# Kernel tuning notes

Measured on AMD Instinct MI355X. Metric: run time of the kernel, lower is better.

## Reference

```python
import jax, jax.numpy as jnp
import numpy as np

B, T, F, U = 256, 2048, 64, 10  # batch, timesteps, features, lstm units


def setup_inputs() -> dict:
    key = jax.random.key(0)
    k1, k2, k3, k4 = jax.random.split(key, 4)
    return {
        "x": jax.random.normal(k1, (B, T, F), dtype=jnp.float32),
        "kernel": jax.random.normal(k2, (F, 4 * U), dtype=jnp.float32) * 0.1,
        "recurrent_kernel": jax.random.normal(k3, (U, 4 * U), dtype=jnp.float32) * 0.1,
        "bias": jnp.zeros((4 * U,), dtype=jnp.float32),
        "dense_w": jax.random.normal(k4, (U, 1), dtype=jnp.float32) * 0.1,
        "dense_b": jnp.zeros((1,), dtype=jnp.float32),
    }


def reference(x, kernel, recurrent_kernel, bias, dense_w, dense_b):
    units = recurrent_kernel.shape[0]
    batch = x.shape[0]
    # Precompute input contribution for all timesteps: [B, T, 4U]
    xz = jnp.einsum('btf,fg->btg', x, kernel) + bias

    def step(carry, z_t):
        h, c = carry
        z = z_t + h @ recurrent_kernel  # [B, 4U]
        i, f, g, o = jnp.split(z, 4, axis=-1)  # Keras gate order: i, f, c, o
        i = jax.nn.sigmoid(i)
        f = jax.nn.sigmoid(f)
        g = jax.nn.soft_sign(g)       # activation='softsign'
        o = jax.nn.sigmoid(o)
        c = f * c + i * g
        h = o * jax.nn.soft_sign(c)
        return (h, c), None

    h0 = jnp.zeros((batch, units), dtype=x.dtype)
    (h, _), _ = jax.lax.scan(step, (h0, h0), jnp.swapaxes(xz, 0, 1))
    logit = h @ dense_w + dense_b  # [B, 1]
    return jax.nn.sigmoid(logit)
```

## Files before the change

### kernel.cpp

```cpp
#include <hip/hip_runtime.h>

#define B_ 256
#define T_ 2048
#define F_ 64
#define U_ 10
#define G_ 40
#define CH 64
#define NCH (T_ / CH)
#define NLOG2E (-1.44269504088896340736f)

__device__ __forceinline__ float rcp_f(float x) { return __builtin_amdgcn_rcpf(x); }
__device__ __forceinline__ float exp2_f(float x) { return __builtin_amdgcn_exp2f(x); }
__device__ __forceinline__ float rdlane_f(float v, int l) {
  return __int_as_float(__builtin_amdgcn_readlane(__float_as_int(v), l));
}
template <int CTRL>
__device__ __forceinline__ float qbcast(float v) {
  return __int_as_float(
      __builtin_amdgcn_update_dpp(0, __float_as_int(v), CTRL, 0xF, 0xF, true));
}
__device__ __forceinline__ void gload_lds16(const float* g, float* l) {
  __builtin_amdgcn_global_load_lds(
      (const __attribute__((address_space(1))) void*)g,
      (__attribute__((address_space(3))) void*)l, 16, 0, 0);
}

__global__ __launch_bounds__(256, 1) void lstm_fused(
    const float* __restrict__ x, const float* __restrict__ W,
    const float* __restrict__ R, const float* __restrict__ bias,
    const float* __restrict__ dw, const float* __restrict__ db,
    float* __restrict__ out) {
  __shared__ float xb[2][CH * F_];
  __shared__ float zb[2][CH * G_];
  const int b = blockIdx.x;
  const int tid = threadIdx.x;
  const int wave = tid >> 6;
  const int lane = tid & 63;
  const float* xbase = x + (size_t)b * T_ * F_;

  if (wave == 0) {
    __builtin_amdgcn_s_setprio(3);
    const int L = (lane < G_) ? lane : (G_ - 1);
    const int u = L >> 2, gate = L & 3;
    const int col = gate * U_ + u;
    const float sc = (gate == 2) ? 1.f : NLOG2E;
    float Rc[U_];
    #pragma unroll
    for (int j = 0; j < U_; ++j) Rc[j] = R[j * G_ + col] * sc;
    const float dwu = dw[u];
    const float db0 = db[0];
    float h = 0.f, c = 0.f;

    auto step = [&](float zseed) {
      float h0 = rdlane_f(h, 0),  h1 = rdlane_f(h, 4),  h2 = rdlane_f(h, 8);
      float h3 = rdlane_f(h, 12), h4 = rdlane_f(h, 16), h5 = rdlane_f(h, 20);
      float h6 = rdlane_f(h, 24), h7 = rdlane_f(h, 28);
      float h8 = rdlane_f(h, 32), h9 = rdlane_f(h, 36);
      float q0 = fmaf(h0, Rc[0], zseed);
      q0 = fmaf(h1, Rc[1], q0);
      q0 = fmaf(h2, Rc[2], q0);
      float q1 = h3 * Rc[3];
      q1 = fmaf(h4, Rc[4], q1);
      q1 = fmaf(h5, Rc[5], q1);
      float q2 = h6 * Rc[6];
      q2 = fmaf(h7, Rc[7], q2);
      float q3 = h8 * Rc[8];
      q3 = fmaf(h9, Rc[9], q3);
      float zz = (q0 + q2) + (q1 + q3);
      float sg = rcp_f(1.f + exp2_f(zz));
      float ss = zz * rcp_f(1.f + __builtin_fabsf(zz));
      float a = (gate == 2) ? ss : sg;
      float ai = qbcast<0x00>(a);
      float af = qbcast<0x55>(a);
      float ag = qbcast<0xAA>(a);
      float ao = qbcast<0xFF>(a);
      c = fmaf(af, c, ai * ag);
      float oc = ao * c;
      float den = 1.f + __builtin_fabsf(c);
      h = oc * rcp_f(den);
    };

    __syncthreads();
    __syncthreads();
    for (int cc = 0; cc < NCH; ++cc) {
      const float* zp = zb[cc & 1] + L;
      float zA0 = zp[0 * G_], zA1 = zp[1 * G_], zA2 = zp[2 * G_], zA3 = zp[3 * G_];
      float zB0 = zp[4 * G_], zB1 = zp[5 * G_], zB2 = zp[6 * G_], zB3 = zp[7 * G_];
      #pragma unroll 1
      for (int pr = 0; pr < 8; ++pr) {
        const float* zn = zp + 8 * G_;
        const float* zs = (pr < 7) ? zn : zp;
        float c0 = zA0, c1 = zA1, c2 = zA2, c3 = zA3;
        zA0 = zs[0 * G_]; zA1 = zs[1 * G_];
        zA2 = zs[2 * G_]; zA3 = zs[3 * G_];
        step(c0); step(c1); step(c2); step(c3);
        float d0 = zB0, d1 = zB1, d2 = zB2, d3 = zB3;
        zB0 = zs[4 * G_]; zB1 = zs[5 * G_];
        zB2 = zs[6 * G_]; zB3 = zs[7 * G_];
        step(d0); step(d1); step(d2); step(d3);
        zp = zn;
      }
      __syncthreads();
    }
    float p = h * dwu;
    float logit = db0;
    #pragma unroll
    for (int j = 0; j < U_; ++j) logit += rdlane_f(p, 4 * j);
    if (lane == 0) out[b] = rcp_f(1.f + __expf(-logit));
  } else {
    const int p0 = tid - 64;
    const int p = (p0 < 160) ? p0 : 159;
    const bool act = (p0 < 160);
    const int s = p % G_;
    const int tsl = p / G_;
    const int u = s >> 2, gate = s & 3;
    const int col = gate * U_ + u;
    const int pw = wave - 1;
    const float scp = (gate == 2) ? 1.f : NLOG2E;
    float wc[F_];
    #pragma unroll
    for (int k = 0; k < F_; ++k) wc[k] = W[k * G_ + col];
    const float bcol = bias[col];

    auto load_x = [&](int cx) {
      const float* g = xbase + (size_t)cx * CH * F_;
      float* l = xb[cx & 1];
      for (int i = pw; i < 16; i += 3)
        gload_lds16(g + i * 256 + lane * 4, l + i * 256);
    };
    auto produce = [&](int tc) {
      const float* xr = xb[tc & 1];
      float* zrow = zb[tc & 1];
      for (int tt = tsl; tt < CH; tt += 4) {
        const float4* row4 = (const float4*)(xr + tt * F_);
        float z0 = bcol, z1 = 0.f, z2 = 0.f, z3 = 0.f;
        #pragma unroll
        for (int j = 0; j < 16; j += 4) {
          float4 a0 = row4[j], a1 = row4[j + 1], a2 = row4[j + 2], a3 = row4[j + 3];
          z0 = fmaf(a0.x, wc[4*j+0], z0);  z0 = fmaf(a0.y, wc[4*j+1], z0);
          z0 = fmaf(a0.z, wc[4*j+2], z0);  z0 = fmaf(a0.w, wc[4*j+3], z0);
          z1 = fmaf(a1.x, wc[4*j+4], z1);  z1 = fmaf(a1.y, wc[4*j+5], z1);
          z1 = fmaf(a1.z, wc[4*j+6], z1);  z1 = fmaf(a1.w, wc[4*j+7], z1);
          z2 = fmaf(a2.x, wc[4*j+8], z2);  z2 = fmaf(a2.y, wc[4*j+9], z2);
          z2 = fmaf(a2.z, wc[4*j+10], z2); z2 = fmaf(a2.w, wc[4*j+11], z2);
          z3 = fmaf(a3.x, wc[4*j+12], z3); z3 = fmaf(a3.y, wc[4*j+13], z3);
          z3 = fmaf(a3.z, wc[4*j+14], z3); z3 = fmaf(a3.w, wc[4*j+15], z3);
        }
        if (act) zrow[tt * G_ + s] = ((z0 + z1) + (z2 + z3)) * scp;
      }
    };

    load_x(0);
    load_x(1);
    __syncthreads();
    produce(0);
    __syncthreads();
    for (int cc = 0; cc < NCH; ++cc) {
      if (cc + 2 < NCH) load_x(cc + 2);
      if (cc + 1 < NCH) produce(cc + 1);
      __syncthreads();
    }
  }
}

extern "C" void kernel_launch(void* const* d_in, const int* in_sizes, int n_in,
                              void* d_out, int out_size, void* d_ws, size_t ws_size,
                              hipStream_t stream) {
  const float* x    = (const float*)d_in[0];
  const float* W    = (const float*)d_in[1];
  const float* R    = (const float*)d_in[2];
  const float* bias = (const float*)d_in[3];
  const float* dw   = (const float*)d_in[4];
  const float* db   = (const float*)d_in[5];
  float* out = (float*)d_out;
  (void)d_ws; (void)ws_size; (void)in_sizes; (void)n_in; (void)out_size;
  lstm_fused<<<B_, 256, 0, stream>>>(x, W, R, bias, dw, db, out);
}
```

Measured before the change: 358.6 us.

## Process two batch sequences per block to interleave independent recurrences

```diff
diff --git a/kernel.cpp b/kernel.cpp
--- a/kernel.cpp
+++ b/kernel.cpp
@@ -5,7 +5,7 @@
 #define F_ 64
 #define U_ 10
 #define G_ 40
-#define CH 64
+#define CH 32
 #define NCH (T_ / CH)
 #define NLOG2E (-1.44269504088896340736f)
 
@@ -30,13 +30,14 @@
     const float* __restrict__ R, const float* __restrict__ bias,
     const float* __restrict__ dw, const float* __restrict__ db,
     float* __restrict__ out) {
-  __shared__ float xb[2][CH * F_];
-  __shared__ float zb[2][CH * G_];
-  const int b = blockIdx.x;
+  __shared__ float xb[2][2][CH * F_];
+  __shared__ float2 zbuf[2][CH * G_];
+  const int blk = blockIdx.x;
   const int tid = threadIdx.x;
   const int wave = tid >> 6;
   const int lane = tid & 63;
-  const float* xbase = x + (size_t)b * T_ * F_;
+  const float* xA = x + (size_t)(2 * blk) * T_ * F_;
+  const float* xBp = x + (size_t)(2 * blk + 1) * T_ * F_;
 
   if (wave == 0) {
     __builtin_amdgcn_s_setprio(3);
@@ -49,64 +50,81 @@
     for (int j = 0; j < U_; ++j) Rc[j] = R[j * G_ + col] * sc;
     const float dwu = dw[u];
     const float db0 = db[0];
-    float h = 0.f, c = 0.f;
-
-    auto step = [&](float zseed) {
-      float h0 = rdlane_f(h, 0),  h1 = rdlane_f(h, 4),  h2 = rdlane_f(h, 8);
-      float h3 = rdlane_f(h, 12), h4 = rdlane_f(h, 16), h5 = rdlane_f(h, 20);
-      float h6 = rdlane_f(h, 24), h7 = rdlane_f(h, 28);
-      float h8 = rdlane_f(h, 32), h9 = rdlane_f(h, 36);
-      float q0 = fmaf(h0, Rc[0], zseed);
-      q0 = fmaf(h1, Rc[1], q0);
-      q0 = fmaf(h2, Rc[2], q0);
-      float q1 = h3 * Rc[3];
-      q1 = fmaf(h4, Rc[4], q1);
-      q1 = fmaf(h5, Rc[5], q1);
-      float q2 = h6 * Rc[6];
-      q2 = fmaf(h7, Rc[7], q2);
-      float q3 = h8 * Rc[8];
-      q3 = fmaf(h9, Rc[9], q3);
-      float zz = (q0 + q2) + (q1 + q3);
-      float sg = rcp_f(1.f + exp2_f(zz));
-      float ss = zz * rcp_f(1.f + __builtin_fabsf(zz));
-      float a = (gate == 2) ? ss : sg;
-      float ai = qbcast<0x00>(a);
-      float af = qbcast<0x55>(a);
-      float ag = qbcast<0xAA>(a);
-      float ao = qbcast<0xFF>(a);
-      c = fmaf(af, c, ai * ag);
-      float oc = ao * c;
-      float den = 1.f + __builtin_fabsf(c);
-      h = oc * rcp_f(den);
+    float hA = 0.f, cA = 0.f, hB = 0.f, cB = 0.f;
+
+    auto step2 = [&](float2 z2) {
+      float a0 = rdlane_f(hA, 0),  b0 = rdlane_f(hB, 0);
+      float a1 = rdlane_f(hA, 4),  b1 = rdlane_f(hB, 4);
+      float a2 = rdlane_f(hA, 8),  b2 = rdlane_f(hB, 8);
+      float a3 = rdlane_f(hA, 12), b3 = rdlane_f(hB, 12);
+      float a4 = rdlane_f(hA, 16), b4 = rdlane_f(hB, 16);
+      float a5 = rdlane_f(hA, 20), b5 = rdlane_f(hB, 20);
+      float a6 = rdlane_f(hA, 24), b6 = rdlane_f(hB, 24);
+      float a7 = rdlane_f(hA, 28), b7 = rdlane_f(hB, 28);
+      float a8 = rdlane_f(hA, 32), b8 = rdlane_f(hB, 32);
+      float a9 = rdlane_f(hA, 36), b9 = rdlane_f(hB, 36);
+      float qa0 = fmaf(a0, Rc[0], z2.x);  float qb0 = fmaf(b0, Rc[0], z2.y);
+      qa0 = fmaf(a1, Rc[1], qa0);         qb0 = fmaf(b1, Rc[1], qb0);
+      qa0 = fmaf(a2, Rc[2], qa0);         qb0 = fmaf(b2, Rc[2], qb0);
+      float qa1 = a3 * Rc[3];             float qb1 = b3 * Rc[3];
+      qa1 = fmaf(a4, Rc[4], qa1);         qb1 = fmaf(b4, Rc[4], qb1);
+      qa1 = fmaf(a5, Rc[5], qa1);         qb1 = fmaf(b5, Rc[5], qb1);
+      float qa2 = a6 * Rc[6];             float qb2 = b6 * Rc[6];
+      qa2 = fmaf(a7, Rc[7], qa2);         qb2 = fmaf(b7, Rc[7], qb2);
+      float qa3 = a8 * Rc[8];             float qb3 = b8 * Rc[8];
+      qa3 = fmaf(a9, Rc[9], qa3);         qb3 = fmaf(b9, Rc[9], qb3);
+      float zzA = (qa0 + qa2) + (qa1 + qa3);
+      float zzB = (qb0 + qb2) + (qb1 + qb3);
+      float eA = exp2_f(zzA);             float eB = exp2_f(zzB);
+      float tA = (gate == 2) ? __builtin_fabsf(zzA) : eA;
+      float tB = (gate == 2) ? __builtin_fabsf(zzB) : eB;
+      float rA = rcp_f(1.f + tA);         float rB = rcp_f(1.f + tB);
+      float aAct = (gate == 2) ? zzA * rA : rA;
+      float bAct = (gate == 2) ? zzB * rB : rB;
+      float aiA = qbcast<0x00>(aAct), aiB = qbcast<0x00>(bAct);
+      float afA = qbcast<0x55>(aAct), afB = qbcast<0x55>(bAct);
+      float agA = qbcast<0xAA>(aAct), agB = qbcast<0xAA>(bAct);
+      float aoA = qbcast<0xFF>(aAct), aoB = qbcast<0xFF>(bAct);
+      cA = fmaf(afA, cA, aiA * agA);      cB = fmaf(afB, cB, aiB * agB);
+      float ocA = aoA * cA;               float ocB = aoB * cB;
+      float denA = 1.f + __builtin_fabsf(cA);
+      float denB = 1.f + __builtin_fabsf(cB);
+      hA = ocA * rcp_f(denA);             hB = ocB * rcp_f(denB);
     };
 
     __syncthreads();
     __syncthreads();
     for (int cc = 0; cc < NCH; ++cc) {
-      const float* zp = zb[cc & 1] + L;
-      float zA0 = zp[0 * G_], zA1 = zp[1 * G_], zA2 = zp[2 * G_], zA3 = zp[3 * G_];
-      float zB0 = zp[4 * G_], zB1 = zp[5 * G_], zB2 = zp[6 * G_], zB3 = zp[7 * G_];
+      const float2* zp = zbuf[cc & 1] + L;
+      float2 zA0 = zp[0 * G_], zA1 = zp[1 * G_], zA2 = zp[2 * G_], zA3 = zp[3 * G_];
+      float2 zB0 = zp[4 * G_], zB1 = zp[5 * G_], zB2 = zp[6 * G_], zB3 = zp[7 * G_];
       #pragma unroll 1
-      for (int pr = 0; pr < 8; ++pr) {
-        const float* zn = zp + 8 * G_;
-        const float* zs = (pr < 7) ? zn : zp;
-        float c0 = zA0, c1 = zA1, c2 = zA2, c3 = zA3;
+      for (int pr = 0; pr < 4; ++pr) {
+        const float2* zn = zp + 8 * G_;
+        const float2* zs = (pr < 3) ? zn : zp;
+        float2 s0 = zA0, s1 = zA1, s2 = zA2, s3 = zA3;
         zA0 = zs[0 * G_]; zA1 = zs[1 * G_];
         zA2 = zs[2 * G_]; zA3 = zs[3 * G_];
-        step(c0); step(c1); step(c2); step(c3);
-        float d0 = zB0, d1 = zB1, d2 = zB2, d3 = zB3;
+        step2(s0); step2(s1); step2(s2); step2(s3);
+        float2 d0 = zB0, d1 = zB1, d2 = zB2, d3 = zB3;
         zB0 = zs[4 * G_]; zB1 = zs[5 * G_];
         zB2 = zs[6 * G_]; zB3 = zs[7 * G_];
-        step(d0); step(d1); step(d2); step(d3);
+        step2(d0); step2(d1); step2(d2); step2(d3);
         zp = zn;
       }
       __syncthreads();
     }
-    float p = h * dwu;
-    float logit = db0;
+    float pA = hA * dwu, pB = hB * dwu;
+    float lgA = db0, lgB = db0;
     #pragma unroll
-    for (int j = 0; j < U_; ++j) logit += rdlane_f(p, 4 * j);
-    if (lane == 0) out[b] = rcp_f(1.f + __expf(-logit));
+    for (int j = 0; j < U_; ++j) {
+      lgA += rdlane_f(pA, 4 * j);
+      lgB += rdlane_f(pB, 4 * j);
+    }
+    if (lane == 0) {
+      out[2 * blk] = rcp_f(1.f + __expf(-lgA));
+      out[2 * blk + 1] = rcp_f(1.f + __expf(-lgB));
+    }
   } else {
     const int p0 = tid - 64;
     const int p = (p0 < 160) ? p0 : 159;
@@ -123,30 +141,55 @@
     const float bcol = bias[col];
 
     auto load_x = [&](int cx) {
-      const float* g = xbase + (size_t)cx * CH * F_;
-      float* l = xb[cx & 1];
-      for (int i = pw; i < 16; i += 3)
-        gload_lds16(g + i * 256 + lane * 4, l + i * 256);
+      const size_t co = (size_t)cx * CH * F_;
+      float* ldst = &xb[cx & 1][0][0];
+      for (int i = pw; i < 16; i += 3) {
+        const float* g = (i < 8) ? (xA + co + i * 256 + lane * 4)
+                                 : (xBp + co + (i - 8) * 256 + lane * 4);
+        gload_lds16(g, ldst + i * 256);
+      }
     };
     auto produce = [&](int tc) {
-      const float* xr = xb[tc & 1];
-      float* zrow = zb[tc & 1];
+      const float* xrA = xb[tc & 1][0];
+      const float* xrB = xb[tc & 1][1];
+      float2* zrow = zbuf[tc & 1];
       for (int tt = tsl; tt < CH; tt += 4) {
-        const float4* row4 = (const float4*)(xr + tt * F_);
-        float z0 = bcol, z1 = 0.f, z2 = 0.f, z3 = 0.f;
-        #pragma unroll
-        for (int j = 0; j < 16; j += 4) {
-          float4 a0 = row4[j], a1 = row4[j + 1], a2 = row4[j + 2], a3 = row4[j + 3];
-          z0 = fmaf(a0.x, wc[4*j+0], z0);  z0 = fmaf(a0.y, wc[4*j+1], z0);
-          z0 = fmaf(a0.z, wc[4*j+2], z0);  z0 = fmaf(a0.w, wc[4*j+3], z0);
-          z1 = fmaf(a1.x, wc[4*j+4], z1);  z1 = fmaf(a1.y, wc[4*j+5], z1);
-          z1 = fmaf(a1.z, wc[4*j+6], z1);  z1 = fmaf(a1.w, wc[4*j+7], z1);
-          z2 = fmaf(a2.x, wc[4*j+8], z2);  z2 = fmaf(a2.y, wc[4*j+9], z2);
-          z2 = fmaf(a2.z, wc[4*j+10], z2); z2 = fmaf(a2.w, wc[4*j+11], z2);
-          z3 = fmaf(a3.x, wc[4*j+12], z3); z3 = fmaf(a3.y, wc[4*j+13], z3);
-          z3 = fmaf(a3.z, wc[4*j+14], z3); z3 = fmaf(a3.w, wc[4*j+15], z3);
+        float zA, zB;
+        {
+          const float4* row4 = (const float4*)(xrA + tt * F_);
+          float z0 = bcol, z1 = 0.f, z2 = 0.f, z3 = 0.f;
+          #pragma unroll
+          for (int j = 0; j < 16; j += 4) {
+            float4 a0 = row4[j], a1 = row4[j + 1], a2 = row4[j + 2], a3 = row4[j + 3];
+            z0 = fmaf(a0.x, wc[4*j+0], z0);  z0 = fmaf(a0.y, wc[4*j+1], z0);
+            z0 = fmaf(a0.z, wc[4*j+2], z0);  z0 = fmaf(a0.w, wc[4*j+3], z0);
+            z1 = fmaf(a1.x, wc[4*j+4], z1);  z1 = fmaf(a1.y, wc[4*j+5], z1);
+            z1 = fmaf(a1.z, wc[4*j+6], z1);  z1 = fmaf(a1.w, wc[4*j+7], z1);
+            z2 = fmaf(a2.x, wc[4*j+8], z2);  z2 = fmaf(a2.y, wc[4*j+9], z2);
+            z2 = fmaf(a2.z, wc[4*j+10], z2); z2 = fmaf(a2.w, wc[4*j+11], z2);
+            z3 = fmaf(a3.x, wc[4*j+12], z3); z3 = fmaf(a3.y, wc[4*j+13], z3);
+            z3 = fmaf(a3.z, wc[4*j+14], z3); z3 = fmaf(a3.w, wc[4*j+15], z3);
+          }
+          zA = ((z0 + z1) + (z2 + z3)) * scp;
         }
-        if (act) zrow[tt * G_ + s] = ((z0 + z1) + (z2 + z3)) * scp;
+        {
+          const float4* row4 = (const float4*)(xrB + tt * F_);
+          float z0 = bcol, z1 = 0.f, z2 = 0.f, z3 = 0.f;
+          #pragma unroll
+          for (int j = 0; j < 16; j += 4) {
+            float4 a0 = row4[j], a1 = row4[j + 1], a2 = row4[j + 2], a3 = row4[j + 3];
+            z0 = fmaf(a0.x, wc[4*j+0], z0);  z0 = fmaf(a0.y, wc[4*j+1], z0);
+            z0 = fmaf(a0.z, wc[4*j+2], z0);  z0 = fmaf(a0.w, wc[4*j+3], z0);
+            z1 = fmaf(a1.x, wc[4*j+4], z1);  z1 = fmaf(a1.y, wc[4*j+5], z1);
+            z1 = fmaf(a1.z, wc[4*j+6], z1);  z1 = fmaf(a1.w, wc[4*j+7], z1);
+            z2 = fmaf(a2.x, wc[4*j+8], z2);  z2 = fmaf(a2.y, wc[4*j+9], z2);
+            z2 = fmaf(a2.z, wc[4*j+10], z2); z2 = fmaf(a2.w, wc[4*j+11], z2);
+            z3 = fmaf(a3.x, wc[4*j+12], z3); z3 = fmaf(a3.y, wc[4*j+13], z3);
+            z3 = fmaf(a3.z, wc[4*j+14], z3); z3 = fmaf(a3.w, wc[4*j+15], z3);
+          }
+          zB = ((z0 + z1) + (z2 + z3)) * scp;
+        }
+        if (act) zrow[tt * G_ + s] = make_float2(zA, zB);
       }
     };
 
@@ -174,5 +217,5 @@
   const float* db   = (const float*)d_in[5];
   float* out = (float*)d_out;
   (void)d_ws; (void)ws_size; (void)in_sizes; (void)n_in; (void)out_size;
-  lstm_fused<<<B_, 256, 0, stream>>>(x, W, R, bias, dw, db, out);
-}
+  lstm_fused<<<B_ / 2, 256, 0, stream>>>(x, W, R, bias, dw, db, out);
+}
```

Result: slower. 495.2 us (+38.1%).
